# Optimization experiments

Measured on AMD Instinct MI355X. Metric: run time of the kernel, lower is better.

Reference implementation:

```python
import jax, jax.numpy as jnp
import numpy as np

NUM_ROUTING = 3


def squash(s, axis):
    # v = |s|^2/(1+|s|^2) * s/|s|  (eq. 1 of the CapsNet paper)
    mag_sq = jnp.sum(s * s, axis=axis, keepdims=True)
    mag = jnp.sqrt(mag_sq)
    return mag_sq / (1.0 + mag_sq) * (s / mag)


def setup_inputs() -> dict:
    key = jax.random.key(0)
    k1, k2 = jax.random.split(key)
    B, I, C, U, S = 256, 8, 1152, 10, 16
    x = jax.random.normal(k1, (B, I, C), dtype=jnp.float32)
    weight = jax.random.normal(k2, (1, C, U, S, I), dtype=jnp.float32)
    return {"x": x, "weight": weight}


def reference(x, weight):
    # x: [B, in_unit, in_channel]; weight: [1, C, U, S, I]
    B = x.shape[0]
    C, U = weight.shape[1], weight.shape[2]
    x_t = jnp.transpose(x, (0, 2, 1))  # [B, C, I]
    # u_hat[b,c,u,s] = sum_i W[0,c,u,s,i] * x_t[b,c,i]
    u_hat = jnp.einsum('cusi,bci->bcus', weight[0], x_t)  # [B, C, U, S]

    b_ij = jnp.zeros((1, C, U, 1), dtype=u_hat.dtype)
    # s_j = (c_ij * u_hat).sum(dim=0): c_ij is batch-independent, so
    # precompute the batch-sum once instead of re-broadcasting each iter.
    u_sum = jnp.sum(u_hat, axis=0, keepdims=True)  # [1, C, U, S]

    v_j = None
    for _ in range(NUM_ROUTING):
        c_ij = jax.nn.softmax(b_ij, axis=2)          # [1, C, U, 1]
        s_j = c_ij * u_sum                           # [1, C, U, S]
        v_j = squash(s_j, axis=3)                    # [1, C, U, S]
        # agreement: mean over batch of <u_hat[b,c,u,:], v_j[0,c,u,:]>
        u_vj1 = jnp.einsum('bcus,cus->cu', u_hat, v_j[0]) / B  # [C, U]
        b_ij = b_ij + u_vj1[None, :, :, None]
    return v_j[0]  # squeeze -> [C, U, S]
```

## Files before the change

kernel.cpp:

```cpp
#include <hip/hip_runtime.h>

#define B_DIM 256
#define I_DIM 8
#define C_DIM 1152
#define U_DIM 10
#define S_DIM 16
#define T_DIM (I_DIM * C_DIM)
#define NCHUNK 8

__global__ __launch_bounds__(256) void batch_reduce_kernel(
    const float* __restrict__ x, float* __restrict__ partial) {
    const int t = blockIdx.x * 256 + threadIdx.x;
    const int k = blockIdx.y;
    const float* p = x + (size_t)(k * (B_DIM / NCHUNK)) * T_DIM + t;
    float acc = 0.f;
#pragma unroll
    for (int b = 0; b < B_DIM / NCHUNK; ++b)
        acc += p[(size_t)b * T_DIM];
    partial[k * T_DIM + t] = acc;
}

__global__ __launch_bounds__(64) void routing_kernel(
    const float* __restrict__ partial, const float* __restrict__ W,
    float* __restrict__ out) {
    __shared__ float foldbuf[2][32];
    __shared__ float xs_lds[32];

    const int tid = threadIdx.x;
    const int c0 = blockIdx.x * 4;

    {
        const int p = tid & 31;
        const int grp = tid >> 5;
        const int c_l = p >> 3, ii = p & 7;
        const float* pp = partial + (size_t)grp * 4 * T_DIM + ii * C_DIM + (c0 + c_l);
        float a = 0.f;
#pragma unroll
        for (int k = 0; k < 4; ++k) a += pp[(size_t)k * T_DIM];
        foldbuf[grp][p] = a;
    }
    __syncthreads();
    if (tid < 32) xs_lds[tid] = foldbuf[0][tid] + foldbuf[1][tid];
    __syncthreads();

    const int c_local = tid >> 4;
    const int s = tid & 15;
    const int c = c0 + c_local;

    float xs[I_DIM];
#pragma unroll
    for (int i = 0; i < I_DIM; ++i) xs[i] = xs_lds[c_local * 8 + i];

    float us[U_DIM];
#pragma unroll
    for (int u = 0; u < U_DIM; ++u) {
        const float4* w = (const float4*)(W + (((size_t)c * U_DIM + u) * S_DIM + s) * I_DIM);
        float4 w0 = w[0], w1 = w[1];
        us[u] = w0.x * xs[0] + w0.y * xs[1] + w0.z * xs[2] + w0.w * xs[3] +
                w1.x * xs[4] + w1.y * xs[5] + w1.z * xs[6] + w1.w * xs[7];
    }

    float bij[U_DIM];
    float v[U_DIM];

#pragma unroll
    for (int u = 0; u < U_DIM; ++u) {
        const float sj = 0.1f * us[u];
        float msq = sj * sj;
#pragma unroll
        for (int w = 1; w < 16; w <<= 1) msq += __shfl_xor(msq, w);
        const float vv = (msq / (1.f + msq)) * (sj * __frsqrt_rn(msq) * rsqrtf(msq) * msq) ;
        (void)vv;
        const float mag = sqrtf(msq);
        const float v0 = (msq / (1.f + msq)) * (sj / mag);
        v[u] = v0;
        float a = us[u] * v0;
#pragma unroll
        for (int w = 1; w < 16; w <<= 1) a += __shfl_xor(a, w);
        bij[u] = a * (1.f / (float)B_DIM);
    }

#pragma unroll
    for (int it = 1; it < 3; ++it) {
        float m = bij[0];
#pragma unroll
        for (int u = 1; u < U_DIM; ++u) m = fmaxf(m, bij[u]);
        float e[U_DIM];
        float sum = 0.f;
#pragma unroll
        for (int u = 0; u < U_DIM; ++u) { e[u] = __expf(bij[u] - m); sum += e[u]; }
        const float inv = 1.f / sum;

#pragma unroll
        for (int u = 0; u < U_DIM; ++u) {
            const float sj = e[u] * inv * us[u];
            float msq = sj * sj;
#pragma unroll
            for (int w = 1; w < 16; w <<= 1) msq += __shfl_xor(msq, w);
            const float mag = sqrtf(msq);
            const float vv = (msq / (1.f + msq)) * (sj / mag);
            v[u] = vv;
            if (it < 2) {
                float a = us[u] * vv;
#pragma unroll
                for (int w = 1; w < 16; w <<= 1) a += __shfl_xor(a, w);
                bij[u] += a * (1.f / (float)B_DIM);
            }
        }
    }

#pragma unroll
    for (int u = 0; u < U_DIM; ++u)
        out[(size_t)c * (U_DIM * S_DIM) + u * S_DIM + s] = v[u];
}

extern "C" void kernel_launch(void* const* d_in, const int* in_sizes, int n_in,
                              void* d_out, int out_size, void* d_ws, size_t ws_size,
                              hipStream_t stream) {
    const float* x = (const float*)d_in[0];
    const float* W = (const float*)d_in[1];
    float* out = (float*)d_out;
    float* partial = (float*)d_ws;

    dim3 g1(T_DIM / 256, NCHUNK);
    batch_reduce_kernel<<<g1, 256, 0, stream>>>(x, partial);

    routing_kernel<<<C_DIM / 4, 64, 0, stream>>>(partial, W, out);
}
```

Before: 73.31 us.

## Fuse batch reduction and routing into one kernel with register-prefetched weights

Merges the separate batch-sum kernel and the routing kernel into one launch. Each 256-thread block now covers 16 capsules, reduces x over the batch with float4 loads, and folds the partial sums through shared memory. The weights are loaded into registers before the reduction so their latency overlaps the x reads. This removes the workspace round trip and a kernel launch, but it leaves only 72 blocks to stream x, so there is less parallelism for the memory-bound reduction.

```diff
diff --git a/kernel.cpp b/kernel.cpp
--- a/kernel.cpp
+++ b/kernel.cpp
@@ -5,125 +5,129 @@
 #define C_DIM 1152
 #define U_DIM 10
 #define S_DIM 16
-#define T_DIM (I_DIM * C_DIM)
-#define NCHUNK 8
+#define ROW (I_DIM * C_DIM)
 
-__global__ __launch_bounds__(256) void batch_reduce_kernel(
-    const float* __restrict__ x, float* __restrict__ partial) {
-    const int t = blockIdx.x * 256 + threadIdx.x;
-    const int k = blockIdx.y;
-    const float* p = x + (size_t)(k * (B_DIM / NCHUNK)) * T_DIM + t;
-    float acc = 0.f;
+__global__ __launch_bounds__(256) void capsule_fused(
+    const float* __restrict__ x, const float* __restrict__ W,
+    float* __restrict__ out) {
+  __shared__ float4 fold[256];
+  __shared__ float xs_lds[16][I_DIM];
+
+  const int tid = threadIdx.x;
+  const int c0 = blockIdx.x * 16;
+  const int c_local = tid >> 4;
+  const int s = tid & 15;
+  const int c = c0 + c_local;
+
+  const float4* wp =
+      (const float4*)(W + (size_t)c * (U_DIM * S_DIM * I_DIM) + s * I_DIM);
+  float4 wreg[U_DIM][2];
 #pragma unroll
-    for (int b = 0; b < B_DIM / NCHUNK; ++b)
-        acc += p[(size_t)b * T_DIM];
-    partial[k * T_DIM + t] = acc;
-}
+  for (int u = 0; u < U_DIM; ++u) {
+    wreg[u][0] = wp[u * (S_DIM * I_DIM / 4)];
+    wreg[u][1] = wp[u * (S_DIM * I_DIM / 4) + 1];
+  }
 
-__global__ __launch_bounds__(64) void routing_kernel(
-    const float* __restrict__ partial, const float* __restrict__ W,
-    float* __restrict__ out) {
-    __shared__ float foldbuf[2][32];
-    __shared__ float xs_lds[32];
+  {
+    const int b8 = tid >> 5;
+    const int i = (tid >> 2) & 7;
+    const int cq = tid & 3;
+    const float* p = x + (size_t)(b8 * 32) * ROW + i * C_DIM + c0 + cq * 4;
+    float4 acc = {0.f, 0.f, 0.f, 0.f};
+#pragma unroll 16
+    for (int j = 0; j < 32; ++j) {
+      const float4 v = *(const float4*)(p + (size_t)j * ROW);
+      acc.x += v.x; acc.y += v.y; acc.z += v.z; acc.w += v.w;
+    }
+    fold[tid] = acc;
+  }
+  __syncthreads();
+  if (tid < 32) {
+    float4 a = fold[tid];
+#pragma unroll
+    for (int k = 1; k < 8; ++k) {
+      const float4 v = fold[k * 32 + tid];
+      a.x += v.x; a.y += v.y; a.z += v.z; a.w += v.w;
+    }
+    const int i = tid >> 2, cq = tid & 3;
+    xs_lds[cq * 4 + 0][i] = a.x;
+    xs_lds[cq * 4 + 1][i] = a.y;
+    xs_lds[cq * 4 + 2][i] = a.z;
+    xs_lds[cq * 4 + 3][i] = a.w;
+  }
+  __syncthreads();
 
-    const int tid = threadIdx.x;
-    const int c0 = blockIdx.x * 4;
+  float xs[I_DIM];
+#pragma unroll
+  for (int i = 0; i < I_DIM; ++i) xs[i] = xs_lds[c_local][i];
 
-    {
-        const int p = tid & 31;
-        const int grp = tid >> 5;
-        const int c_l = p >> 3, ii = p & 7;
-        const float* pp = partial + (size_t)grp * 4 * T_DIM + ii * C_DIM + (c0 + c_l);
-        float a = 0.f;
+  float us[U_DIM];
 #pragma unroll
-        for (int k = 0; k < 4; ++k) a += pp[(size_t)k * T_DIM];
-        foldbuf[grp][p] = a;
-    }
-    __syncthreads();
-    if (tid < 32) xs_lds[tid] = foldbuf[0][tid] + foldbuf[1][tid];
-    __syncthreads();
+  for (int u = 0; u < U_DIM; ++u) {
+    const float4 w0 = wreg[u][0], w1 = wreg[u][1];
+    us[u] = w0.x * xs[0] + w0.y * xs[1] + w0.z * xs[2] + w0.w * xs[3] +
+            w1.x * xs[4] + w1.y * xs[5] + w1.z * xs[6] + w1.w * xs[7];
+  }
 
-    const int c_local = tid >> 4;
-    const int s = tid & 15;
-    const int c = c0 + c_local;
+  float bij[U_DIM];
+  float v[U_DIM];
 
-    float xs[I_DIM];
 #pragma unroll
-    for (int i = 0; i < I_DIM; ++i) xs[i] = xs_lds[c_local * 8 + i];
+  for (int u = 0; u < U_DIM; ++u) {
+    const float sj = 0.1f * us[u];
+    float msq = sj * sj;
+#pragma unroll
+    for (int w = 1; w < 16; w <<= 1) msq += __shfl_xor(msq, w);
+    const float mag = sqrtf(msq);
+    const float v0 = (msq / (1.f + msq)) * (sj / mag);
+    v[u] = v0;
+    float a = us[u] * v0;
+#pragma unroll
+    for (int w = 1; w < 16; w <<= 1) a += __shfl_xor(a, w);
+    bij[u] = a * (1.f / (float)B_DIM);
+  }
 
-    float us[U_DIM];
 #pragma unroll
-    for (int u = 0; u < U_DIM; ++u) {
-        const float4* w = (const float4*)(W + (((size_t)c * U_DIM + u) * S_DIM + s) * I_DIM);
-        float4 w0 = w[0], w1 = w[1];
-        us[u] = w0.x * xs[0] + w0.y * xs[1] + w0.z * xs[2] + w0.w * xs[3] +
-                w1.x * xs[4] + w1.y * xs[5] + w1.z * xs[6] + w1.w * xs[7];
-    }
-
-    float bij[U_DIM];
-    float v[U_DIM];
+  for (int it = 1; it < 3; ++it) {
+    float m = bij[0];
+#pragma unroll
+    for (int u = 1; u < U_DIM; ++u) m = fmaxf(m, bij[u]);
+    float e[U_DIM];
+    float sum = 0.f;
+#pragma unroll
+    for (int u = 0; u < U_DIM; ++u) { e[u] = __expf(bij[u] - m); sum += e[u]; }
+    const float inv = 1.f / sum;
 
 #pragma unroll
     for (int u = 0; u < U_DIM; ++u) {
-        const float sj = 0.1f * us[u];
-        float msq = sj * sj;
+      const float sj = e[u] * inv * us[u];
+      float msq = sj * sj;
 #pragma unroll
-        for (int w = 1; w < 16; w <<= 1) msq += __shfl_xor(msq, w);
-        const float vv = (msq / (1.f + msq)) * (sj * __frsqrt_rn(msq) * rsqrtf(msq) * msq) ;
-        (void)vv;
-        const float mag = sqrtf(msq);
-        const float v0 = (msq / (1.f + msq)) * (sj / mag);
-        v[u] = v0;
-        float a = us[u] * v0;
+      for (int w = 1; w < 16; w <<= 1) msq += __shfl_xor(msq, w);
+      const float mag = sqrtf(msq);
+      const float vv = (msq / (1.f + msq)) * (sj / mag);
+      v[u] = vv;
+      if (it < 2) {
+        float a = us[u] * vv;
 #pragma unroll
         for (int w = 1; w < 16; w <<= 1) a += __shfl_xor(a, w);
-        bij[u] = a * (1.f / (float)B_DIM);
+        bij[u] += a * (1.f / (float)B_DIM);
+      }
     }
+  }
 
 #pragma unroll
-    for (int it = 1; it < 3; ++it) {
-        float m = bij[0];
-#pragma unroll
-        for (int u = 1; u < U_DIM; ++u) m = fmaxf(m, bij[u]);
-        float e[U_DIM];
-        float sum = 0.f;
-#pragma unroll
-        for (int u = 0; u < U_DIM; ++u) { e[u] = __expf(bij[u] - m); sum += e[u]; }
-        const float inv = 1.f / sum;
-
-#pragma unroll
-        for (int u = 0; u < U_DIM; ++u) {
-            const float sj = e[u] * inv * us[u];
-            float msq = sj * sj;
-#pragma unroll
-            for (int w = 1; w < 16; w <<= 1) msq += __shfl_xor(msq, w);
-            const float mag = sqrtf(msq);
-            const float vv = (msq / (1.f + msq)) * (sj / mag);
-            v[u] = vv;
-            if (it < 2) {
-                float a = us[u] * vv;
-#pragma unroll
-                for (int w = 1; w < 16; w <<= 1) a += __shfl_xor(a, w);
-                bij[u] += a * (1.f / (float)B_DIM);
-            }
-        }
-    }
-
-#pragma unroll
-    for (int u = 0; u < U_DIM; ++u)
-        out[(size_t)c * (U_DIM * S_DIM) + u * S_DIM + s] = v[u];
+  for (int u = 0; u < U_DIM; ++u)
+    out[(size_t)c * (U_DIM * S_DIM) + u * S_DIM + s] = v[u];
 }
 
 extern "C" void kernel_launch(void* const* d_in, const int* in_sizes, int n_in,
                               void* d_out, int out_size, void* d_ws, size_t ws_size,
                               hipStream_t stream) {
-    const float* x = (const float*)d_in[0];
-    const float* W = (const float*)d_in[1];
-    float* out = (float*)d_out;
-    float* partial = (float*)d_ws;
+  const float* x = (const float*)d_in[0];
+  const float* W = (const float*)d_in[1];
+  float* out = (float*)d_out;
+  (void)d_ws; (void)ws_size;
 
-    dim3 g1(T_DIM / 256, NCHUNK);
-    batch_reduce_kernel<<<g1, 256, 0, stream>>>(x, partial);
-
-    routing_kernel<<<C_DIM / 4, 64, 0, stream>>>(partial, W, out);
+  capsule_fused<<<dim3(C_DIM / 16), 256, 0, stream>>>(x, W, out);
 }
```

Result: slower. 78.30 us (+6.8%).
